# Kernel tuning notes

Measured on AMD Instinct MI355X. Metric: run time of the kernel, lower is better.

## Reference

```python
import math
import jax, jax.numpy as jnp
import numpy as np

EMBED_DIM = 512
NUM_CLASSES = 100000
NUM_SUBCENTERS = 3
MARGIN = 0.5
SCALE = 64.0
BATCH = 256


def setup_inputs() -> dict:
    key = jax.random.key(0)
    k1, k2, k3 = jax.random.split(key, 3)
    embeddings = jax.random.normal(k1, (BATCH, EMBED_DIM), dtype=jnp.float32)
    labels = jax.random.randint(k2, (BATCH,), 0, NUM_CLASSES, dtype=jnp.int64)
    # xavier_uniform for (C*K, D): bound = sqrt(6/(fan_in+fan_out))
    fan_out, fan_in = NUM_CLASSES * NUM_SUBCENTERS, EMBED_DIM
    bound = math.sqrt(6.0 / (fan_in + fan_out))
    weight = jax.random.uniform(k3, (fan_out, fan_in), dtype=jnp.float32,
                                minval=-bound, maxval=bound)
    return {"embeddings": embeddings, "labels": labels, "weight": weight}


def reference(embeddings, labels, weight):
    eps = 1e-12
    cos_m = math.cos(MARGIN)
    sin_m = math.sin(MARGIN)
    th = math.cos(math.pi - MARGIN)
    mm = math.sin(math.pi - MARGIN) * MARGIN

    # L2 normalize (matches F.normalize with eps clamp on norm)
    e = embeddings / jnp.maximum(jnp.linalg.norm(embeddings, axis=-1, keepdims=True), eps)
    w = weight / jnp.maximum(jnp.linalg.norm(weight, axis=-1, keepdims=True), eps)

    # (N, C*K) cosine, class-major / subcenter-minor ordering like torch .view
    cosine_all = jnp.einsum('nd,md->nm', e, w).reshape(-1, NUM_CLASSES, NUM_SUBCENTERS)
    cosine = jnp.max(cosine_all, axis=2)                       # (N, C)

    sine = jnp.sqrt(jnp.clip(1.0 - jnp.square(cosine), 0.0, 1.0))
    phi = cosine * cos_m - sine * sin_m
    phi = jnp.where(cosine > th, phi, cosine - mm)

    one_hot = jax.nn.one_hot(labels, NUM_CLASSES, dtype=cosine.dtype)  # (N, C)
    logits = SCALE * (one_hot * phi + (1.0 - one_hot) * cosine)

    # mean cross entropy
    logz = jax.nn.logsumexp(logits, axis=-1)                   # (N,)
    label_logit = jnp.take_along_axis(logits, labels[:, None], axis=-1)[:, 0]
    return jnp.mean(logz - label_logit)
```

## Files before the change

### kernel.cpp

```cpp
#include <hip/hip_runtime.h>
#include <hip/hip_bf16.h>
#include <math.h>

#define EMBED_DIM 512
#define NUM_CLASSES 100000
#define NUM_SUB 3
#define BATCH 256
#define M_TOTAL (NUM_CLASSES*NUM_SUB)
#define BM 48
#define BK 64
#define LDB 72
#define NBLOCKS (M_TOTAL/BM)

typedef float  floatx4 __attribute__((ext_vector_type(4)));
typedef __bf16 bf16x8  __attribute__((ext_vector_type(8)));

__device__ __forceinline__ unsigned int f2bf(float f){
  unsigned int u = __float_as_uint(f);
  u += 0x7FFFu + ((u >> 16) & 1u);
  return u >> 16;
}

__global__ __launch_bounds__(64) void normalize_pack(
    const float* __restrict__ E, unsigned short* __restrict__ ehat)
{
  const int r    = blockIdx.x;
  const int lane = threadIdx.x;
  const float4 v0 = *(const float4*)(E + r*EMBED_DIM + lane*8);
  const float4 v1 = *(const float4*)(E + r*EMBED_DIM + lane*8 + 4);
  float ssq = v0.x*v0.x + v0.y*v0.y + v0.z*v0.z + v0.w*v0.w
            + v1.x*v1.x + v1.y*v1.y + v1.z*v1.z + v1.w*v1.w;
  #pragma unroll
  for (int m = 1; m < 64; m <<= 1) ssq += __shfl_xor(ssq, m, 64);
  float nn = sqrtf(ssq);
  nn = fmaxf(nn, 1e-12f);
  const float rn = 1.0f / nn;
  const float vals[8] = {v0.x, v0.y, v0.z, v0.w, v1.x, v1.y, v1.z, v1.w};
  unsigned int p[4];
  #pragma unroll
  for (int i = 0; i < 4; ++i)
    p[i] = f2bf(vals[2*i]*rn) | (f2bf(vals[2*i+1]*rn) << 16);
  const int kt = lane >> 3;
  const size_t off = (size_t)kt*(BATCH*BK) + (size_t)r*BK + (lane & 7)*8;
  *(uint4*)(ehat + off) = make_uint4(p[0], p[1], p[2], p[3]);
}

__global__ __launch_bounds__(256, 3) void arcface_main(
    const float* __restrict__ W,
    const unsigned short* __restrict__ ehat,
    const int* __restrict__ labels,
    float* __restrict__ gsum,
    float* __restrict__ llogit)
{
  __builtin_assume(threadIdx.x < 256);
  __shared__ char  smem[13824];
  __shared__ float snorm[BM];

  const int tid  = threadIdx.x;
  const int wave = tid >> 6, lane = tid & 63;
  const int m0   = blockIdx.x * BM;
  const int r16  = tid >> 4, c4 = tid & 15;
  const int col  = lane & 15, quad = lane >> 4;

  unsigned short* tile = (unsigned short*)smem;

  floatx4 acc[12] = {};
  float ssq_acc[3] = {0,0,0};

  const unsigned short* abase = ehat + (wave*64 + col)*64 + quad*8;
  const float* wbase = W + (size_t)m0*EMBED_DIM + c4*4;

  bf16x8 a[4][2];
  float4 bv[2][3];

  #pragma unroll
  for (int i = 0; i < 3; ++i)
    bv[0][i] = *(const float4*)(wbase + (size_t)(i*16 + r16)*EMBED_DIM);
  #pragma unroll
  for (int i = 0; i < 3; ++i)
    bv[1][i] = *(const float4*)(wbase + (size_t)(i*16 + r16)*EMBED_DIM + BK);
  #pragma unroll
  for (int rt = 0; rt < 4; ++rt)
    #pragma unroll
    for (int h = 0; h < 2; ++h)
      a[rt][h] = *(const bf16x8*)(abase + rt*1024 + h*32);
  {
    unsigned short* tw = tile;
    #pragma unroll
    for (int i = 0; i < 3; ++i){
      const float4 v = bv[0][i];
      ssq_acc[i] += v.x*v.x + v.y*v.y + v.z*v.z + v.w*v.w;
      const int row = i*16 + r16;
      *(uint2*)(tw + row*LDB + c4*4) =
          make_uint2(f2bf(v.x) | (f2bf(v.y) << 16), f2bf(v.z) | (f2bf(v.w) << 16));
    }
  }
  __syncthreads();

  #pragma unroll
  for (int s = 0; s < 8; ++s){
    if (s < 6){
      #pragma unroll
      for (int i = 0; i < 3; ++i)
        bv[s & 1][i] = *(const float4*)(wbase + (size_t)(i*16 + r16)*EMBED_DIM + (s+2)*BK);
    }
    if (s < 7){
      unsigned short* tw = tile + ((s+1) & 1)*(48*LDB);
      #pragma unroll
      for (int i = 0; i < 3; ++i){
        const float4 v = bv[(s+1) & 1][i];
        ssq_acc[i] += v.x*v.x + v.y*v.y + v.z*v.z + v.w*v.w;
        const int row = i*16 + r16;
        *(uint2*)(tw + row*LDB + c4*4) =
            make_uint2(f2bf(v.x) | (f2bf(v.y) << 16), f2bf(v.z) | (f2bf(v.w) << 16));
      }
    }
    {
      const unsigned short* tr = tile + (s & 1)*(48*LDB);
      #pragma unroll
      for (int h = 0; h < 2; ++h){
        bf16x8 b[3];
        #pragma unroll
        for (int ct = 0; ct < 3; ++ct)
          b[ct] = *(const bf16x8*)(tr + (ct*16 + col)*LDB + h*32 + quad*8);
        #pragma unroll
        for (int rt = 0; rt < 4; ++rt)
          #pragma unroll
          for (int ct = 0; ct < 3; ++ct)
            acc[rt*3 + ct] = __builtin_amdgcn_mfma_f32_16x16x32_bf16(
                a[rt][h], b[ct], acc[rt*3 + ct], 0, 0, 0);
      }
    }
    if (s < 7){
      #pragma unroll
      for (int rt = 0; rt < 4; ++rt)
        #pragma unroll
        for (int h = 0; h < 2; ++h)
          a[rt][h] = *(const bf16x8*)(abase + (s+1)*16384 + rt*1024 + h*32);
    }
    __syncthreads();
  }

  #pragma unroll
  for (int it = 0; it < 3; ++it){
    float s = ssq_acc[it];
    s += __shfl_xor(s, 1, 64); s += __shfl_xor(s, 2, 64);
    s += __shfl_xor(s, 4, 64); s += __shfl_xor(s, 8, 64);
    if (c4 == 0) snorm[it*16 + r16] = s;
  }
  __syncthreads();

  float rnorm3[3];
  #pragma unroll
  for (int i = 0; i < 3; ++i){
    float nw = sqrtf(snorm[i*16 + col]);
    rnorm3[i] = 1.0f / fmaxf(nw, 1e-12f);
  }
  float* ebuf = (float*)smem + wave*(16*49);
  const int cls0 = m0 / 3;
  const float cos_m = 0.87758256189037276f;
  const float sin_m = 0.47942553860420301f;
  const float thr   = -0.87758256189037276f;
  const float mmv   = 0.23971276930210156f;

  #pragma unroll
  for (int rt = 0; rt < 4; ++rt){
    #pragma unroll
    for (int ct = 0; ct < 3; ++ct)
      #pragma unroll
      for (int r = 0; r < 4; ++r)
        ebuf[(quad*4 + r)*49 + ct*16 + col] = acc[rt*3 + ct][r] * rnorm3[ct];
    __syncthreads();
    if (quad == 0){
      const int brow = wave*64 + rt*16 + col;
      const int lbl  = labels[brow];
      float contrib = 0.0f;
      for (int c = 0; c < 16; ++c){
        const float a0 = ebuf[col*49 + 3*c + 0];
        const float a1 = ebuf[col*49 + 3*c + 1];
        const float a2 = ebuf[col*49 + 3*c + 2];
        float cm = fmaxf(a0, fmaxf(a1, a2));
        float val = cm;
        if (cls0 + c == lbl){
          const float sine = sqrtf(fmaxf(0.0f, 1.0f - cm*cm));
          const float phi  = cm*cos_m - sine*sin_m;
          val = (cm > thr) ? phi : (cm - mmv);
          llogit[brow] = 64.0f * val;
        }
        contrib += __expf(64.0f*val - 64.0f);
      }
      atomicAdd(&gsum[brow*16], contrib);
    }
    __syncthreads();
  }
}

__global__ __launch_bounds__(256) void finalize_loss(
    const float* __restrict__ gsum, const float* __restrict__ llogit,
    float* __restrict__ out)
{
  const int tid = threadIdx.x;
  float v = logf(gsum[tid*16]) + 64.0f - llogit[tid];
  #pragma unroll
  for (int m = 1; m < 64; m <<= 1) v += __shfl_xor(v, m, 64);
  __shared__ float red[4];
  if ((tid & 63) == 0) red[tid >> 6] = v;
  __syncthreads();
  if (tid == 0) out[0] = (red[0] + red[1] + red[2] + red[3]) * (1.0f/BATCH);
}

extern "C" void kernel_launch(void* const* d_in, const int* in_sizes, int n_in,
                              void* d_out, int out_size, void* d_ws, size_t ws_size,
                              hipStream_t stream)
{
  const float* emb    = (const float*)d_in[0];
  const int*   labels = (const int*)d_in[1];
  const float* W      = (const float*)d_in[2];

  unsigned short* ehat   = (unsigned short*)d_ws;
  float*          gsum   = (float*)((char*)d_ws + 262144);
  float*          llogit = (float*)((char*)d_ws + 262144 + 16384);

  hipMemsetAsync(gsum, 0, 16384, stream);
  normalize_pack<<<BATCH, 64, 0, stream>>>(emb, ehat);
  arcface_main<<<NBLOCKS, 256, 0, stream>>>(W, ehat, labels, gsum, llogit);
  finalize_loss<<<1, 256, 0, stream>>>(gsum, llogit, (float*)d_out);
}
```

Baseline: 960.0 us.

## Load W straight into MFMA B registers per wave, dropping LDS staging

Each wave now loads its own fp32 weight fragments from global memory directly into the MFMA B-operand layout. It converts them to bf16 in registers and accumulates row sum-of-squares there, replacing the shared-memory tile and the per-stage __syncthreads. The weight norm reduction becomes cross-lane shuffles instead of going through shared memory. The trade-off is that all four waves redundantly fetch the same W tile, roughly quadrupling L1/L2 request traffic. Register pressure also rises, and the launch bound moves to 2 blocks per SIMD.

```diff
diff --git a/kernel.cpp b/kernel.cpp
--- a/kernel.cpp
+++ b/kernel.cpp
@@ -8,8 +8,6 @@
 #define BATCH 256
 #define M_TOTAL (NUM_CLASSES*NUM_SUB)
 #define BM 48
-#define BK 64
-#define LDB 72
 #define NBLOCKS (M_TOTAL/BM)
 
 typedef float  floatx4 __attribute__((ext_vector_type(4)));
@@ -41,122 +39,114 @@
   for (int i = 0; i < 4; ++i)
     p[i] = f2bf(vals[2*i]*rn) | (f2bf(vals[2*i+1]*rn) << 16);
   const int kt = lane >> 3;
-  const size_t off = (size_t)kt*(BATCH*BK) + (size_t)r*BK + (lane & 7)*8;
+  const size_t off = (size_t)kt*(BATCH*64) + (size_t)r*64 + (lane & 7)*8;
   *(uint4*)(ehat + off) = make_uint4(p[0], p[1], p[2], p[3]);
 }
 
-__global__ __launch_bounds__(256, 3) void arcface_main(
+__global__ __launch_bounds__(256, 2) void arcface_main(
     const float* __restrict__ W,
     const unsigned short* __restrict__ ehat,
     const int* __restrict__ labels,
     float* __restrict__ gsum,
     float* __restrict__ llogit)
 {
-  __builtin_assume(threadIdx.x < 256);
-  __shared__ char  smem[13824];
-  __shared__ float snorm[BM];
+  __shared__ float ebuf_all[4*16*49];
 
   const int tid  = threadIdx.x;
   const int wave = tid >> 6, lane = tid & 63;
+  const int col  = lane & 15, quad = lane >> 4;
   const int m0   = blockIdx.x * BM;
-  const int r16  = tid >> 4, c4 = tid & 15;
-  const int col  = lane & 15, quad = lane >> 4;
-
-  unsigned short* tile = (unsigned short*)smem;
 
   floatx4 acc[12] = {};
-  float ssq_acc[3] = {0,0,0};
+  float   ssq[3]  = {0,0,0};
 
   const unsigned short* abase = ehat + (wave*64 + col)*64 + quad*8;
-  const float* wbase = W + (size_t)m0*EMBED_DIM + c4*4;
-
-  bf16x8 a[4][2];
-  float4 bv[2][3];
-
-  #pragma unroll
-  for (int i = 0; i < 3; ++i)
-    bv[0][i] = *(const float4*)(wbase + (size_t)(i*16 + r16)*EMBED_DIM);
-  #pragma unroll
-  for (int i = 0; i < 3; ++i)
-    bv[1][i] = *(const float4*)(wbase + (size_t)(i*16 + r16)*EMBED_DIM + BK);
-  #pragma unroll
-  for (int rt = 0; rt < 4; ++rt)
-    #pragma unroll
-    for (int h = 0; h < 2; ++h)
-      a[rt][h] = *(const bf16x8*)(abase + rt*1024 + h*32);
-  {
-    unsigned short* tw = tile;
-    #pragma unroll
-    for (int i = 0; i < 3; ++i){
-      const float4 v = bv[0][i];
-      ssq_acc[i] += v.x*v.x + v.y*v.y + v.z*v.z + v.w*v.w;
-      const int row = i*16 + r16;
-      *(uint2*)(tw + row*LDB + c4*4) =
-          make_uint2(f2bf(v.x) | (f2bf(v.y) << 16), f2bf(v.z) | (f2bf(v.w) << 16));
-    }
+  const float* wrow[3];
+  #pragma unroll
+  for (int ct = 0; ct < 3; ++ct)
+    wrow[ct] = W + (size_t)(m0 + ct*16 + col)*EMBED_DIM + quad*8;
+
+  float4 fvA[3][2][2], fvB[3][2][2];
+  bf16x8 a[4][2], b[3][2];
+
+#define LOADW(dst, ktv) do {                                              \
+    _Pragma("unroll")                                                     \
+    for (int ct = 0; ct < 3; ++ct){                                       \
+      const float* wp = wrow[ct] + (ktv)*64;                              \
+      _Pragma("unroll")                                                   \
+      for (int h = 0; h < 2; ++h){                                        \
+        dst[ct][h][0] = *(const float4*)(wp + h*32);                      \
+        dst[ct][h][1] = *(const float4*)(wp + h*32 + 4);                  \
+      }                                                                   \
+    }                                                                     \
+  } while(0)
+
+#define CONVB(src) do {                                                   \
+    _Pragma("unroll")                                                     \
+    for (int ct = 0; ct < 3; ++ct){                                       \
+      _Pragma("unroll")                                                   \
+      for (int h = 0; h < 2; ++h){                                        \
+        const float4 v0 = src[ct][h][0], v1 = src[ct][h][1];              \
+        ssq[ct] += v0.x*v0.x + v0.y*v0.y + v0.z*v0.z + v0.w*v0.w          \
+                 + v1.x*v1.x + v1.y*v1.y + v1.z*v1.z + v1.w*v1.w;         \
+        union { uint4 u; bf16x8 h8; } cv;                                 \
+        cv.u = make_uint4(f2bf(v0.x) | (f2bf(v0.y) << 16),                \
+                          f2bf(v0.z) | (f2bf(v0.w) << 16),                \
+                          f2bf(v1.x) | (f2bf(v1.y) << 16),                \
+                          f2bf(v1.z) | (f2bf(v1.w) << 16));               \
+        b[ct][h] = cv.h8;                                                 \
+      }                                                                   \
+    }                                                                     \
+  } while(0)
+
+#define LOADA(ktv) do {                                                   \
+    _Pragma("unroll")                                                     \
+    for (int rt = 0; rt < 4; ++rt)                                        \
+      _Pragma("unroll")                                                   \
+      for (int h = 0; h < 2; ++h)                                         \
+        a[rt][h] = *(const bf16x8*)(abase + (ktv)*16384 + rt*1024 + h*32);\
+  } while(0)
+
+#define MFMAS() do {                                                      \
+    _Pragma("unroll")                                                     \
+    for (int h = 0; h < 2; ++h)                                           \
+      _Pragma("unroll")                                                   \
+      for (int rt = 0; rt < 4; ++rt)                                      \
+        _Pragma("unroll")                                                 \
+        for (int ct = 0; ct < 3; ++ct)                                    \
+          acc[rt*3 + ct] = __builtin_amdgcn_mfma_f32_16x16x32_bf16(       \
+              a[rt][h], b[ct][h], acc[rt*3 + ct], 0, 0, 0);               \
+  } while(0)
+
+  LOADW(fvA, 0);
+  LOADW(fvB, 1);
+
+  #pragma unroll 1
+  for (int kt = 0; kt < 8; kt += 2){
+    LOADA(kt);
+    CONVB(fvA);
+    if (kt + 2 < 8) LOADW(fvA, kt + 2);
+    MFMAS();
+    LOADA(kt + 1);
+    CONVB(fvB);
+    if (kt + 3 < 8) LOADW(fvB, kt + 3);
+    MFMAS();
   }
-  __syncthreads();
-
-  #pragma unroll
-  for (int s = 0; s < 8; ++s){
-    if (s < 6){
-      #pragma unroll
-      for (int i = 0; i < 3; ++i)
-        bv[s & 1][i] = *(const float4*)(wbase + (size_t)(i*16 + r16)*EMBED_DIM + (s+2)*BK);
-    }
-    if (s < 7){
-      unsigned short* tw = tile + ((s+1) & 1)*(48*LDB);
-      #pragma unroll
-      for (int i = 0; i < 3; ++i){
-        const float4 v = bv[(s+1) & 1][i];
-        ssq_acc[i] += v.x*v.x + v.y*v.y + v.z*v.z + v.w*v.w;
-        const int row = i*16 + r16;
-        *(uint2*)(tw + row*LDB + c4*4) =
-            make_uint2(f2bf(v.x) | (f2bf(v.y) << 16), f2bf(v.z) | (f2bf(v.w) << 16));
-      }
-    }
-    {
-      const unsigned short* tr = tile + (s & 1)*(48*LDB);
-      #pragma unroll
-      for (int h = 0; h < 2; ++h){
-        bf16x8 b[3];
-        #pragma unroll
-        for (int ct = 0; ct < 3; ++ct)
-          b[ct] = *(const bf16x8*)(tr + (ct*16 + col)*LDB + h*32 + quad*8);
-        #pragma unroll
-        for (int rt = 0; rt < 4; ++rt)
-          #pragma unroll
-          for (int ct = 0; ct < 3; ++ct)
-            acc[rt*3 + ct] = __builtin_amdgcn_mfma_f32_16x16x32_bf16(
-                a[rt][h], b[ct], acc[rt*3 + ct], 0, 0, 0);
-      }
-    }
-    if (s < 7){
-      #pragma unroll
-      for (int rt = 0; rt < 4; ++rt)
-        #pragma unroll
-        for (int h = 0; h < 2; ++h)
-          a[rt][h] = *(const bf16x8*)(abase + (s+1)*16384 + rt*1024 + h*32);
-    }
-    __syncthreads();
+#undef LOADW
+#undef CONVB
+#undef LOADA
+#undef MFMAS
+
+  float rnorm3[3];
+  #pragma unroll
+  for (int ct = 0; ct < 3; ++ct){
+    float s = ssq[ct];
+    s += __shfl_xor(s, 16, 64);
+    s += __shfl_xor(s, 32, 64);
+    rnorm3[ct] = 1.0f / fmaxf(sqrtf(s), 1e-12f);
   }
 
-  #pragma unroll
-  for (int it = 0; it < 3; ++it){
-    float s = ssq_acc[it];
-    s += __shfl_xor(s, 1, 64); s += __shfl_xor(s, 2, 64);
-    s += __shfl_xor(s, 4, 64); s += __shfl_xor(s, 8, 64);
-    if (c4 == 0) snorm[it*16 + r16] = s;
-  }
-  __syncthreads();
-
-  float rnorm3[3];
-  #pragma unroll
-  for (int i = 0; i < 3; ++i){
-    float nw = sqrtf(snorm[i*16 + col]);
-    rnorm3[i] = 1.0f / fmaxf(nw, 1e-12f);
-  }
-  float* ebuf = (float*)smem + wave*(16*49);
+  float* ebuf = ebuf_all + wave*(16*49);
   const int cls0 = m0 / 3;
   const float cos_m = 0.87758256189037276f;
   const float sin_m = 0.47942553860420301f;
```

New measurement: 1.369 ms. +42.6%, slower.
